# Optimization experiments

Hardware: AMD Instinct MI355X
Metric: run time of the kernel (lower is better)

The kernel has to match this reference:

```python
import jax, jax.numpy as jnp
import numpy as np

FORWARD_STEPS = 50
DT = 0.01
G = 9.81
BATCH = 131072


def _rot(psi):
    # batched 6x6 block-rotation matrix R(psi)
    b = psi.shape[0]
    c, s = jnp.cos(psi), jnp.sin(psi)
    R = jnp.zeros((b, 6, 6), dtype=psi.dtype)
    R = R.at[:, 0, 0].set(c).at[:, 0, 2].set(-s)
    R = R.at[:, 1, 1].set(c).at[:, 1, 3].set(-s)
    R = R.at[:, 2, 0].set(s).at[:, 2, 2].set(c)
    R = R.at[:, 3, 1].set(s).at[:, 3, 3].set(c)
    R = R.at[:, 4, 4].set(1.0).at[:, 5, 5].set(1.0)
    return R


def setup_inputs() -> dict:
    key = jax.random.key(0)
    k1, k2, k3, k4, k5 = jax.random.split(key, 5)
    b = BATCH
    # build initial full state [b, 1, 8]: keep body-frame Vx away from 0 (A divides by Vx)
    fs = jnp.zeros((b, 8), dtype=jnp.float32)
    fs = fs.at[:, 0].set(jax.random.normal(k1, (b,)) * 0.1)                     # x
    fs = fs.at[:, 1].set(jax.random.uniform(k2, (b,), minval=0.5, maxval=1.5))  # x_dot
    fs = fs.at[:, 2].set(jax.random.normal(k3, (b,)) * 0.1)                     # y
    fs = fs.at[:, 3].set(jax.random.uniform(k4, (b,), minval=-0.2, maxval=0.2)) # y_dot
    fs = fs.at[:, 4].set(jax.random.uniform(k5, (b,), minval=-0.3, maxval=0.3)) # psi
    fs = fs.at[:, 5].set(jax.random.normal(jax.random.fold_in(key, 10), (b,)) * 0.1)  # psi_dot
    fs = fs.at[:, 6].set(jax.random.normal(jax.random.fold_in(key, 11), (b,)) * 0.1)  # accel cmd
    fs = fs.at[:, 7].set(jax.random.uniform(jax.random.fold_in(key, 12), (b,), minval=-0.2, maxval=0.2))  # steer cmd
    full_states = fs[:, None, :]
    actions = jnp.stack([
        jax.random.normal(jax.random.fold_in(key, 20), (b, FORWARD_STEPS)) * 0.1,
        jax.random.uniform(jax.random.fold_in(key, 21), (b, FORWARD_STEPS), minval=-0.2, maxval=0.2),
    ], axis=-1).astype(jnp.float32)
    m = 0.2
    return {
        "full_states": full_states,
        "actions": actions,
        "m": jnp.float32(m),
        "Caf": jnp.float32(5 * 0.25 * m * G),
        "Car": jnp.float32(5 * 0.25 * m * G),
        "lf": jnp.float32(0.05),
        "lr": jnp.float32(0.05),
        "Iz": jnp.float32((0.1 ** 2 + 0.1 ** 2) / 12.0),
    }


def reference(full_states, actions, m, Caf, Car, lf, lr, Iz):
    bsz = full_states.shape[0]
    dt = jnp.asarray(DT, dtype=full_states.dtype)
    state0 = full_states[:, -1, :6]   # [b,6]
    action0 = full_states[:, -1, 6:]  # [b,2]
    acts = jnp.transpose(actions, (1, 0, 2))  # [T,b,2]

    def step(carry, a_next):
        s, u = carry
        psi = s[:, 4]
        Vx = s[:, 1] * jnp.cos(psi) + s[:, 3] * jnp.sin(psi)
        A = jnp.zeros((bsz, 6, 6), dtype=s.dtype)
        A = A.at[:, 0, 1].set(1.0).at[:, 2, 3].set(1.0).at[:, 4, 5].set(1.0)
        A = A.at[:, 3, 3].set(-(2 * Caf + 2 * Car) / (m * Vx))
        A = A.at[:, 3, 5].set(-Vx - (2 * Caf * lf - 2 * Car * lr) / (m * Vx))
        A = A.at[:, 5, 3].set(-(2 * lf * Caf - 2 * lr * Car) / (Iz * Vx))
        A = A.at[:, 5, 4].set(-(2 * lf ** 2 * Caf + 2 * lr ** 2 * Car) / (Iz * Vx))
        Bm = jnp.zeros((bsz, 6, 2), dtype=s.dtype)
        Bm = Bm.at[:, 1, 0].set(1.0)
        Bm = Bm.at[:, 3, 1].set(2 * Caf / m)
        Bm = Bm.at[:, 5, 1].set(2 * lf * Caf / Iz)
        s_body = jnp.einsum('bij,bj->bi', _rot(-psi), s)
        temp = jnp.einsum('bij,bj->bi', A, s_body) + jnp.einsum('bij,bj->bi', Bm, u)
        pred = s + jnp.einsum('bij,bj->bi', _rot(psi), temp) * dt
        out = jnp.concatenate([pred, a_next], axis=1)  # [b,8]
        return (pred, a_next), out

    _, outs = jax.lax.scan(step, (state0, action0), acts)
    return jnp.transpose(outs, (1, 0, 2))  # [b, forward_steps, 8]
```

## Files before the change

kernel.cpp:

```cpp
#include <hip/hip_runtime.h>

#define DT 0.01f
#define ROW 18

__global__ __launch_bounds__(256) void hybrid_sim_kernel(
    const float* __restrict__ fs,
    const float* __restrict__ actions,
    const float* __restrict__ pm,  const float* __restrict__ pCaf,
    const float* __restrict__ pCar, const float* __restrict__ plf,
    const float* __restrict__ plr, const float* __restrict__ pIz,
    float* __restrict__ out)
{
    __shared__ float lds[4 * 64 * ROW];

    const int tid  = threadIdx.x;
    const int lane = tid & 63;
    const int wv   = tid >> 6;
    const int b    = blockIdx.x * 256 + tid;
    const int b0w  = blockIdx.x * 256 + (wv << 6);

    const float4* fsp = (const float4*)(fs + (size_t)b * 8);
    float4 f0 = fsp[0];
    float4 f1 = fsp[1];
    float s0=f0.x, s1=f0.y, s2=f0.z, s3=f0.w, s4=f1.x, s5=f1.y, u0=f1.z, u1=f1.w;

    float m=*pm, Caf=*pCaf, Car=*pCar, lf=*plf, lr=*plr, Iz=*pIz;
    float k1  = 2.f*(Caf+Car)/m;
    float k2  = 2.f*(Caf*lf-Car*lr)/m;
    float k3  = 2.f*(lf*Caf-lr*Car)/Iz;
    float k4  = 2.f*(lf*lf*Caf+lr*lr*Car)/Iz;
    float b31 = 2.f*Caf/m;
    float b51 = 2.f*lf*Caf/Iz;

    const float4* ap = (const float4*)(actions + (size_t)b * 100);
    float4 abuf[25];
    #pragma unroll
    for (int j = 0; j < 25; ++j) abuf[j] = ap[j];
    const float* av = (const float*)abuf;

    float* buf = &lds[wv * 64 * ROW];
    float o[16];

    #pragma unroll
    for (int g = 0; g < 25; ++g) {
        #pragma unroll
        for (int hh = 0; hh < 2; ++hh) {
            int tt = g*2 + hh;
            float psi = s4;
            float c  = __cosf(psi);
            float sn = __sinf(psi);
            float Vx  = c*s1 + sn*s3;
            float sb3 = c*s3 - sn*s1;
            float inv = __builtin_amdgcn_rcpf(Vx);
            float t3 = -k1*inv*sb3 + (-Vx - k2*inv)*s5 + b31*u1;
            float t5 = -k3*inv*sb3 - k4*inv*psi + b51*u1;
            float p0 = s0 + DT*(c*Vx - sn*sb3);
            float p2 = s2 + DT*(sn*Vx + c*sb3);
            float p1 = s1 + DT*(c*u0 - sn*t3);
            float p3 = s3 + DT*(sn*u0 + c*t3);
            float p4 = s4 + DT*s5;
            float p5 = s5 + DT*t5;
            float nu0 = av[2*tt];
            float nu1 = av[2*tt+1];
            float* oo = &o[hh*8];
            oo[0]=p0; oo[1]=p1; oo[2]=p2; oo[3]=p3;
            oo[4]=p4; oo[5]=p5; oo[6]=nu0; oo[7]=nu1;
            s0=p0; s1=p1; s2=p2; s3=p3; s4=p4; s5=p5; u0=nu0; u1=nu1;
        }

        float2* rw = (float2*)(buf + lane*ROW);
        #pragma unroll
        for (int j = 0; j < 8; ++j) rw[j] = make_float2(o[2*j], o[2*j+1]);

        #pragma unroll
        for (int k = 0; k < 8; ++k) {
            int e  = k*8 + (lane >> 3);
            int mm = lane & 7;
            float2 v = *(const float2*)(buf + e*ROW + mm*2);
            float2* dst = (float2*)(out + (size_t)(b0w + e)*400 + g*16 + mm*2);
            *dst = v;
        }
    }
}

extern "C" void kernel_launch(void* const* d_in, const int* in_sizes, int n_in,
                              void* d_out, int out_size, void* d_ws, size_t ws_size,
                              hipStream_t stream) {
    const float* fs      = (const float*)d_in[0];
    const float* actions = (const float*)d_in[1];
    int batch = in_sizes[0] / 8;
    int grid  = batch / 256;
    hybrid_sim_kernel<<<grid, 256, 0, stream>>>(
        fs, actions,
        (const float*)d_in[2], (const float*)d_in[3], (const float*)d_in[4],
        (const float*)d_in[5], (const float*)d_in[6], (const float*)d_in[7],
        (float*)d_out);
}
```

Baseline: 302.7 us.

## Widen LDS transpose to float4 with XOR swizzle and software-pipeline stores

The LDS staging transpose now uses 16-byte accesses with an XOR-swizzled slot layout and a padded row of 20 floats, replacing 8-byte accesses. Output stores are 16 bytes wide. Each group's tile is written to LDS after compute and read back at the start of the next group, so its global stores overlap the next group's arithmetic. Action loads are split into five chunks issued across the loop to cut live registers, and launch bounds request two blocks per CU. The extra register-held tile and the swizzle arithmetic could offset the gains.

```diff
diff --git a/kernel.cpp b/kernel.cpp
--- a/kernel.cpp
+++ b/kernel.cpp
@@ -1,9 +1,9 @@
 #include <hip/hip_runtime.h>
 
 #define DT 0.01f
-#define ROW 18
+#define ROW 20
 
-__global__ __launch_bounds__(256) void hybrid_sim_kernel(
+__global__ __launch_bounds__(256, 2) void hybrid_sim_kernel(
     const float* __restrict__ fs,
     const float* __restrict__ actions,
     const float* __restrict__ pm,  const float* __restrict__ pCaf,
@@ -11,7 +11,7 @@
     const float* __restrict__ plr, const float* __restrict__ pIz,
     float* __restrict__ out)
 {
-    __shared__ float lds[4 * 64 * ROW];
+    __shared__ __align__(16) float lds[4 * 64 * ROW];
 
     const int tid  = threadIdx.x;
     const int lane = tid & 63;
@@ -35,17 +35,36 @@
     const float4* ap = (const float4*)(actions + (size_t)b * 100);
     float4 abuf[25];
     #pragma unroll
-    for (int j = 0; j < 25; ++j) abuf[j] = ap[j];
-    const float* av = (const float*)abuf;
+    for (int j = 0; j < 5; ++j) abuf[j] = ap[j];
 
     float* buf = &lds[wv * 64 * ROW];
-    float o[16];
+    const int sw    = (lane >> 3) & 3;
+    const int re_q  = lane >> 2;
+    const int re_mm = lane & 3;
+
+    float4 o4[4];
+    float4 r[4];
 
     #pragma unroll
     for (int g = 0; g < 25; ++g) {
+        if ((g % 5) == 0 && (g / 5 + 1) < 5) {
+            const int c = g / 5 + 1;
+            #pragma unroll
+            for (int j = 0; j < 5; ++j) abuf[c*5 + j] = ap[c*5 + j];
+        }
+
+        if (g > 0) {
+            #pragma unroll
+            for (int k = 0; k < 4; ++k) {
+                const int e    = k*16 + re_q;
+                const int slot = re_mm ^ ((e >> 3) & 3);
+                r[k] = *(const float4*)(buf + e*ROW + slot*4);
+            }
+        }
+
+        const float4 a4 = abuf[g];
         #pragma unroll
         for (int hh = 0; hh < 2; ++hh) {
-            int tt = g*2 + hh;
             float psi = s4;
             float c  = __cosf(psi);
             float sn = __sinf(psi);
@@ -60,26 +79,33 @@
             float p3 = s3 + DT*(sn*u0 + c*t3);
             float p4 = s4 + DT*s5;
             float p5 = s5 + DT*t5;
-            float nu0 = av[2*tt];
-            float nu1 = av[2*tt+1];
-            float* oo = &o[hh*8];
-            oo[0]=p0; oo[1]=p1; oo[2]=p2; oo[3]=p3;
-            oo[4]=p4; oo[5]=p5; oo[6]=nu0; oo[7]=nu1;
+            float nu0 = hh ? a4.z : a4.x;
+            float nu1 = hh ? a4.w : a4.y;
+            o4[hh*2 + 0] = make_float4(p0, p1, p2, p3);
+            o4[hh*2 + 1] = make_float4(p4, p5, nu0, nu1);
             s0=p0; s1=p1; s2=p2; s3=p3; s4=p4; s5=p5; u0=nu0; u1=nu1;
         }
 
-        float2* rw = (float2*)(buf + lane*ROW);
-        #pragma unroll
-        for (int j = 0; j < 8; ++j) rw[j] = make_float2(o[2*j], o[2*j+1]);
+        if (g > 0) {
+            #pragma unroll
+            for (int k = 0; k < 4; ++k) {
+                const int e = k*16 + re_q;
+                *(float4*)(out + (size_t)(b0w + e)*400 + (g-1)*16 + re_mm*4) = r[k];
+            }
+        }
 
         #pragma unroll
-        for (int k = 0; k < 8; ++k) {
-            int e  = k*8 + (lane >> 3);
-            int mm = lane & 7;
-            float2 v = *(const float2*)(buf + e*ROW + mm*2);
-            float2* dst = (float2*)(out + (size_t)(b0w + e)*400 + g*16 + mm*2);
-            *dst = v;
+        for (int j = 0; j < 4; ++j) {
+            *(float4*)(buf + lane*ROW + (j ^ sw)*4) = o4[j];
         }
+    }
+
+    #pragma unroll
+    for (int k = 0; k < 4; ++k) {
+        const int e    = k*16 + re_q;
+        const int slot = re_mm ^ ((e >> 3) & 3);
+        float4 v = *(const float4*)(buf + e*ROW + slot*4);
+        *(float4*)(out + (size_t)(b0w + e)*400 + 24*16 + re_mm*4) = v;
     }
 }
 
```

After: 362.6 us. 19.8% more time.
